# Kernel optimization log

Measured on AMD Instinct MI355X. Metric: run time of the kernel, lower is better.

## Reference

```python
import jax, jax.numpy as jnp
import numpy as np

B, S, D = 2, 2048, 1024
H, DH = 16, 64
EPS = 1e-5

def setup_inputs() -> dict:
    key = jax.random.key(0)
    ks = jax.random.split(key, 8)
    s = 0.02
    return {
        "x": jax.random.normal(ks[0], (B, S, D), dtype=jnp.float32),
        "ln_gamma": jnp.ones((D,), jnp.float32),
        "ln_beta": jnp.zeros((D,), jnp.float32),
        "wq": jax.random.normal(ks[1], (D, H * DH), jnp.float32) * s,
        "bq": jnp.zeros((H * DH,), jnp.float32),
        "wk": jax.random.normal(ks[2], (D, H * DH), jnp.float32) * s,
        "bk": jnp.zeros((H * DH,), jnp.float32),
        "wv": jax.random.normal(ks[3], (D, H * DH), jnp.float32) * s,
        "bv": jnp.zeros((H * DH,), jnp.float32),
        "wo": jax.random.normal(ks[4], (H * DH, D), jnp.float32) * s,
        "bo": jnp.zeros((D,), jnp.float32),
    }

def reference(x, ln_gamma, ln_beta, wq, bq, wk, bk, wv, bv, wo, bo):
    # Pre-LayerNorm over d_model
    mu = jnp.mean(x, axis=-1, keepdims=True)
    var = jnp.var(x, axis=-1, keepdims=True)
    xn = (x - mu) * jax.lax.rsqrt(var + EPS) * ln_gamma + ln_beta

    b, s, _ = xn.shape
    q = (xn @ wq + bq).reshape(b, s, H, DH)
    k = (xn @ wk + bk).reshape(b, s, H, DH)
    v = (xn @ wv + bv).reshape(b, s, H, DH)

    scale = jnp.sqrt(jnp.float32(DH))
    scores = jnp.einsum('bihd,bjhd->bhij', q, k) / scale  # [b,h,s,s]
    att = jax.nn.softmax(scores, axis=-1)
    out = jnp.einsum('bhij,bjhd->bihd', att, v).reshape(b, s, H * DH)
    return out @ wo + bo
```

## Files before the change

kernel.cpp:

```cpp
#include <hip/hip_runtime.h>
#include <math.h>

#define SEQ   2048
#define DM    1024
#define NHEAD 16
#define HD    64
#define NTOK  4096
#define EPS   1e-5f
#define SCALE_C 0.18033688f

typedef __attribute__((ext_vector_type(8))) short v8s;
typedef __attribute__((ext_vector_type(4))) float v4f;
typedef unsigned short ushort_t;

#define GLOAD16(g, l) __builtin_amdgcn_global_load_lds( \
    (const __attribute__((address_space(1))) unsigned int*)(g), \
    (__attribute__((address_space(3))) unsigned int*)(l), 16, 0, 0)

__device__ __forceinline__ unsigned short f2bf(float f) {
  union { float f; unsigned u; } v; v.f = f;
  unsigned r = v.u + 0x7FFFu + ((v.u >> 16) & 1u);
  return (unsigned short)(r >> 16);
}

__device__ __forceinline__ unsigned pack2_bf16(float a, float b) {
  union { float f; unsigned u; } ua, ub;
  ua.f = a; ub.f = b;
  return __builtin_amdgcn_perm(ub.u + 0x8000u, ua.u + 0x8000u, 0x07060302u);
}

__global__ __launch_bounds__(256) void ln_kernel(
    const float* __restrict__ x, const float* __restrict__ g,
    const float* __restrict__ be, ushort_t* __restrict__ y) {
  const int row = blockIdx.x;
  const int t = threadIdx.x;
  const float4 v = ((const float4*)(x + (size_t)row * DM))[t];
  float s  = v.x + v.y + v.z + v.w;
  float ss = v.x*v.x + v.y*v.y + v.z*v.z + v.w*v.w;
  #pragma unroll
  for (int off = 32; off > 0; off >>= 1) {
    s  += __shfl_down(s,  off, 64);
    ss += __shfl_down(ss, off, 64);
  }
  __shared__ float red[8];
  __shared__ float mu_s, rs_s;
  const int wid = t >> 6, lane = t & 63;
  if (lane == 0) { red[wid] = s; red[4 + wid] = ss; }
  __syncthreads();
  if (t == 0) {
    const float S  = red[0] + red[1] + red[2] + red[3];
    const float SS = red[4] + red[5] + red[6] + red[7];
    const float mu  = S * (1.0f / DM);
    const float var = SS * (1.0f / DM) - mu * mu;
    mu_s = mu; rs_s = rsqrtf(var + EPS);
  }
  __syncthreads();
  const float mu = mu_s, r = rs_s;
  const float4 gv = ((const float4*)g)[t];
  const float4 bv = ((const float4*)be)[t];
  ushort4 o;
  o.x = f2bf((v.x - mu) * r * gv.x + bv.x);
  o.y = f2bf((v.y - mu) * r * gv.y + bv.y);
  o.z = f2bf((v.z - mu) * r * gv.z + bv.z);
  o.w = f2bf((v.w - mu) * r * gv.w + bv.w);
  *(ushort4*)(y + (size_t)row * DM + t * 4) = o;
}

__global__ __launch_bounds__(256) void wt_kernel(
    const float* __restrict__ w0, const float* __restrict__ w1,
    const float* __restrict__ w2, const float* __restrict__ w3,
    ushort_t* __restrict__ o0, ushort_t* __restrict__ o1,
    ushort_t* __restrict__ o2, ushort_t* __restrict__ o3) {
  const int z = blockIdx.z;
  const float* w = (z==0) ? w0 : (z==1) ? w1 : (z==2) ? w2 : w3;
  ushort_t* o    = (z==0) ? o0 : (z==1) ? o1 : (z==2) ? o2 : o3;
  __shared__ float tile[64][65];
  const int t = threadIdx.x;
  const int n0 = blockIdx.x * 64, k0 = blockIdx.y * 64;
  const int r = t >> 4, c4 = (t & 15) * 4;
  #pragma unroll
  for (int i = 0; i < 4; ++i) {
    const float4 v = *(const float4*)(w + (size_t)(k0 + r + i*16) * DM + n0 + c4);
    tile[r + i*16][c4 + 0] = v.x;
    tile[r + i*16][c4 + 1] = v.y;
    tile[r + i*16][c4 + 2] = v.z;
    tile[r + i*16][c4 + 3] = v.w;
  }
  __syncthreads();
  #pragma unroll
  for (int i = 0; i < 4; ++i) {
    const int n = r + i*16;
    ushort4 o4;
    o4.x = f2bf(tile[c4 + 0][n]);
    o4.y = f2bf(tile[c4 + 1][n]);
    o4.z = f2bf(tile[c4 + 2][n]);
    o4.w = f2bf(tile[c4 + 3][n]);
    *(ushort4*)(o + (size_t)(n0 + n) * DM + k0 + c4) = o4;
  }
}

__device__ __forceinline__ void gemm_main(ushort_t* lsa, ushort_t* lsb,
    const ushort_t* A, const ushort_t* WT, int m0, int n0, v4f acc[4][4]) {
  const int tid = threadIdx.x;
  const int wid = tid >> 6, lane = tid & 63;
  const int mh = (wid & 1) << 6, nh = (wid >> 1) << 6;
  const int r16 = lane & 15, quad = lane >> 4;
  const int srow = lane >> 2, sch = lane & 3;
  for (int k0 = 0; k0 < DM; k0 += 32) {
    __syncthreads();
    #pragma unroll
    for (int j = 0; j < 2; ++j) {
      const int o = wid * 2 + j;
      GLOAD16(A  + (size_t)(m0 + o*16 + srow) * DM + k0 + sch*8, lsa + o*512);
      GLOAD16(WT + (size_t)(n0 + o*16 + srow) * DM + k0 + sch*8, lsb + o*512);
    }
    __syncthreads();
    v8s af[4], bfr[4];
    #pragma unroll
    for (int i = 0; i < 4; ++i) {
      af[i]  = *(const v8s*)(lsa + (mh + i*16 + r16)*32 + quad*8);
      bfr[i] = *(const v8s*)(lsb + (nh + i*16 + r16)*32 + quad*8);
    }
    #pragma unroll
    for (int i = 0; i < 4; ++i)
      #pragma unroll
      for (int j = 0; j < 4; ++j)
        acc[i][j] = __builtin_amdgcn_mfma_f32_16x16x32_bf16(af[i], bfr[j], acc[i][j], 0, 0, 0);
  }
}

__global__ __launch_bounds__(256, 2) void gemm_qkv(const ushort_t* __restrict__ xn,
    const ushort_t* __restrict__ wtq, const ushort_t* __restrict__ wtk, const ushort_t* __restrict__ wtv,
    const float* __restrict__ bq, const float* __restrict__ bk, const float* __restrict__ bv,
    ushort_t* __restrict__ qo, ushort_t* __restrict__ ko, ushort_t* __restrict__ vto) {
  __shared__ ushort_t lsa[128*32];
  __shared__ ushort_t lsb[128*32];
  const int z = blockIdx.z;
  const ushort_t* WT = (z == 0) ? wtq : (z == 1) ? wtk : wtv;
  const float* bias  = (z == 0) ? bq  : (z == 1) ? bk  : bv;
  const int m0 = blockIdx.y * 128, n0 = blockIdx.x * 128;
  v4f acc[4][4];
  #pragma unroll
  for (int i = 0; i < 4; ++i)
    #pragma unroll
    for (int j = 0; j < 4; ++j) acc[i][j] = (v4f){0.f, 0.f, 0.f, 0.f};
  gemm_main(lsa, lsb, xn, WT, m0, n0, acc);
  const int tid = threadIdx.x, wid = tid >> 6, lane = tid & 63;
  const int mh = (wid & 1) << 6, nh = (wid >> 1) << 6;
  const int r16 = lane & 15, quad = lane >> 4;
  if (z < 2) {
    ushort_t* out = (z == 0) ? qo : ko;
    const float sc = (z == 0) ? SCALE_C : 1.0f;
    #pragma unroll
    for (int bn = 0; bn < 4; ++bn) {
      const int col = n0 + nh + bn*16 + r16;
      const float bb = bias[col];
      #pragma unroll
      for (int am = 0; am < 4; ++am) {
        const int tb = m0 + mh + am*16 + quad*4;
        #pragma unroll
        for (int r = 0; r < 4; ++r)
          out[(size_t)(tb + r) * DM + col] = f2bf((acc[am][bn][r] + bb) * sc);
      }
    }
  } else {
    #pragma unroll
    for (int bn = 0; bn < 4; ++bn) {
      const int col = n0 + nh + bn*16 + r16;
      const float bb = bias[col];
      const int h = col >> 6, d = col & 63;
      #pragma unroll
      for (int am = 0; am < 4; ++am) {
        const int tb = m0 + mh + am*16 + quad*4;
        const int b = tb >> 11, t = tb & 2047;
        ushort4 o4;
        o4.x = f2bf(acc[am][bn][0] + bb);
        o4.y = f2bf(acc[am][bn][1] + bb);
        o4.z = f2bf(acc[am][bn][2] + bb);
        o4.w = f2bf(acc[am][bn][3] + bb);
        *(ushort4*)(vto + ((size_t)(b*NHEAD + h) * HD + d) * SEQ + t) = o4;
      }
    }
  }
}

__global__ __launch_bounds__(256, 2) void gemm_out(const ushort_t* __restrict__ A,
    const ushort_t* __restrict__ WT, const float* __restrict__ bias,
    float* __restrict__ out) {
  __shared__ ushort_t lsa[128*32];
  __shared__ ushort_t lsb[128*32];
  const int m0 = blockIdx.y * 128, n0 = blockIdx.x * 128;
  v4f acc[4][4];
  #pragma unroll
  for (int i = 0; i < 4; ++i)
    #pragma unroll
    for (int j = 0; j < 4; ++j) acc[i][j] = (v4f){0.f, 0.f, 0.f, 0.f};
  gemm_main(lsa, lsb, A, WT, m0, n0, acc);
  const int tid = threadIdx.x, wid = tid >> 6, lane = tid & 63;
  const int mh = (wid & 1) << 6, nh = (wid >> 1) << 6;
  const int r16 = lane & 15, quad = lane >> 4;
  #pragma unroll
  for (int bn = 0; bn < 4; ++bn) {
    const int col = n0 + nh + bn*16 + r16;
    const float bb = bias[col];
    #pragma unroll
    for (int am = 0; am < 4; ++am) {
      const int tb = m0 + mh + am*16 + quad*4;
      #pragma unroll
      for (int r = 0; r < 4; ++r)
        out[(size_t)(tb + r) * DM + col] = acc[am][bn][r] + bb;
    }
  }
}

__global__ __launch_bounds__(256, 4) void attn_kernel(
    const ushort_t* __restrict__ Q, const ushort_t* __restrict__ K,
    const ushort_t* __restrict__ Vt, ushort_t* __restrict__ O) {
  __shared__ ushort_t kbuf[2][8*512];
  __shared__ ushort_t vbuf[2][8*512];
  __shared__ ushort_t pbuf[8*512];
  const int tid = threadIdx.x, wid = tid >> 6, lane = tid & 63;
  const int r16 = lane & 15, quad = lane >> 4;
  const int q0 = blockIdx.x * 64, bh = blockIdx.y;
  const int b = bh >> 4, h = bh & 15;
  const ushort_t* gQ = Q + (size_t)b * SEQ * DM + h * HD;
  const ushort_t* gK = K + (size_t)b * SEQ * DM + h * HD;
  const ushort_t* gV = Vt + (size_t)bh * HD * SEQ;

  auto stage = [&](int kt, int buf) {
    const int k0 = kt * 64;
    if (wid < 2) {
      #pragma unroll
      for (int j = 0; j < 4; ++j) {
        const int o = (wid & 1) * 4 + j;
        GLOAD16(gK + (size_t)(k0 + (o >> 1) * 16 + r16) * DM + (o & 1) * 32 + quad * 8,
                &kbuf[buf][o * 512]);
      }
    } else {
      #pragma unroll
      for (int j = 0; j < 4; ++j) {
        const int o = (wid & 1) * 4 + j;
        GLOAD16(gV + (size_t)((o & 3) * 16 + r16) * SEQ + k0 + (o >> 2) * 32 + quad * 8,
                &vbuf[buf][o * 512]);
      }
    }
  };

  v8s qfr[4][2];
  #pragma unroll
  for (int qa = 0; qa < 4; ++qa) {
    const ushort_t* p = gQ + (size_t)(q0 + qa*16 + r16) * DM + quad * 8;
    qfr[qa][0] = *(const v8s*)p;
    qfr[qa][1] = *(const v8s*)(p + 32);
  }
  v4f acco[4];
  #pragma unroll
  for (int i = 0; i < 4; ++i) acco[i] = (v4f){0.f, 0.f, 0.f, 0.f};
  float lrun[4] = {0.f, 0.f, 0.f, 0.f};

  const int pwoff = ((wid & 1) * 2 + (quad >> 1)) * 128 + r16 * 8 + (quad & 1) * 4;
  const int pblk0 = (wid >> 1) * 512;

  stage(0, 0);
  __syncthreads();

  for (int kt = 0; kt < SEQ / 64; ++kt) {
    const int cur = kt & 1, nxt = cur ^ 1;
    if (kt + 1 < SEQ / 64) stage(kt + 1, nxt);

    const v8s ka0 = *(const v8s*)(&kbuf[cur][(wid*2 + 0) * 512] + lane * 8);
    const v8s ka1 = *(const v8s*)(&kbuf[cur][(wid*2 + 1) * 512] + lane * 8);
    v4f sacc[4];
    #pragma unroll
    for (int qa = 0; qa < 4; ++qa) {
      sacc[qa] = (v4f){0.f, 0.f, 0.f, 0.f};
      sacc[qa] = __builtin_amdgcn_mfma_f32_16x16x32_bf16(ka0, qfr[qa][0], sacc[qa], 0, 0, 0);
      sacc[qa] = __builtin_amdgcn_mfma_f32_16x16x32_bf16(ka1, qfr[qa][1], sacc[qa], 0, 0, 0);
    }

    #pragma unroll
    for (int qa = 0; qa < 4; ++qa) {
      const float e0 = __builtin_amdgcn_exp2f(sacc[qa][0]);
      const float e1 = __builtin_amdgcn_exp2f(sacc[qa][1]);
      const float e2 = __builtin_amdgcn_exp2f(sacc[qa][2]);
      const float e3 = __builtin_amdgcn_exp2f(sacc[qa][3]);
      float ls = (e0 + e1) + (e2 + e3);
      ls += __shfl_xor(ls, 16, 64);
      ls += __shfl_xor(ls, 32, 64);
      lrun[qa] += ls;
      uint2 d2;
      d2.x = pack2_bf16(e0, e1);
      d2.y = pack2_bf16(e2, e3);
      *(uint2*)(pbuf + (qa*2) * 512 + pblk0 + pwoff) = d2;
    }

    __syncthreads();

    const v8s vf0 = *(const v8s*)(&vbuf[cur][(0*4 + wid) * 512] + lane * 8);
    const v8s vf1 = *(const v8s*)(&vbuf[cur][(1*4 + wid) * 512] + lane * 8);
    #pragma unroll
    for (int qa = 0; qa < 4; ++qa) {
      const v8s pb0 = *(const v8s*)(pbuf + (qa*2 + 0) * 512 + lane * 8);
      const v8s pb1 = *(const v8s*)(pbuf + (qa*2 + 1) * 512 + lane * 8);
      acco[qa] = __builtin_amdgcn_mfma_f32_16x16x32_bf16(vf0, pb0, acco[qa], 0, 0, 0);
      acco[qa] = __builtin_amdgcn_mfma_f32_16x16x32_bf16(vf1, pb1, acco[qa], 0, 0, 0);
    }

    __syncthreads();
  }

  float* lred = (float*)pbuf;
  if (quad == 0) {
    #pragma unroll
    for (int qa = 0; qa < 4; ++qa) lred[wid*64 + qa*16 + r16] = lrun[qa];
  }
  __syncthreads();
  ushort_t* gO = O + (size_t)b * SEQ * DM + h * HD;
  #pragma unroll
  for (int qa = 0; qa < 4; ++qa) {
    const int q = qa*16 + r16;
    const float inv = 1.f / ((lred[0*64 + q] + lred[1*64 + q]) + (lred[2*64 + q] + lred[3*64 + q]));
    ushort4 o4;
    o4.x = f2bf(acco[qa][0] * inv);
    o4.y = f2bf(acco[qa][1] * inv);
    o4.z = f2bf(acco[qa][2] * inv);
    o4.w = f2bf(acco[qa][3] * inv);
    *(ushort4*)(gO + (size_t)(q0 + q) * DM + wid*16 + quad*4) = o4;
  }
}

extern "C" void kernel_launch(void* const* d_in, const int* in_sizes, int n_in,
                              void* d_out, int out_size, void* d_ws, size_t ws_size,
                              hipStream_t stream) {
  const float* x     = (const float*)d_in[0];
  const float* gamma = (const float*)d_in[1];
  const float* beta  = (const float*)d_in[2];
  const float* wq    = (const float*)d_in[3];
  const float* bq    = (const float*)d_in[4];
  const float* wk    = (const float*)d_in[5];
  const float* bk    = (const float*)d_in[6];
  const float* wv    = (const float*)d_in[7];
  const float* bv    = (const float*)d_in[8];
  const float* wo    = (const float*)d_in[9];
  const float* bo    = (const float*)d_in[10];
  float* out = (float*)d_out;

  unsigned char* w8 = (unsigned char*)d_ws;
  const size_t MB = 1024 * 1024;
  ushort_t* xn  = (ushort_t*)(w8 + 0 * MB);
  ushort_t* qb  = (ushort_t*)(w8 + 8 * MB);
  ushort_t* kb  = (ushort_t*)(w8 + 16 * MB);
  ushort_t* vt  = (ushort_t*)(w8 + 24 * MB);
  ushort_t* wtq = (ushort_t*)(w8 + 32 * MB);
  ushort_t* wtk = (ushort_t*)(w8 + 34 * MB);
  ushort_t* wtv = (ushort_t*)(w8 + 36 * MB);
  ushort_t* wto = (ushort_t*)(w8 + 38 * MB);
  ushort_t* ob  = xn;

  ln_kernel<<<dim3(NTOK), dim3(256), 0, stream>>>(x, gamma, beta, xn);
  wt_kernel<<<dim3(16, 16, 4), dim3(256), 0, stream>>>(wq, wk, wv, wo, wtq, wtk, wtv, wto);
  gemm_qkv<<<dim3(8, 32, 3), dim3(256), 0, stream>>>(xn, wtq, wtk, wtv, bq, bk, bv, qb, kb, vt);
  attn_kernel<<<dim3(SEQ / 64, 2 * NHEAD), dim3(256), 0, stream>>>(qb, kb, vt, ob);
  gemm_out<<<dim3(8, 32, 1), dim3(256), 0, stream>>>(ob, wto, bo, out);
}
```

Measured before the change: 221.3 us.

## Merge LN and weight prep kernels, drop attention double buffering, raise GEMM occupancy

Merges the LayerNorm and weight-transpose kernels into one launch to save a kernel launch. Raises the GEMM launch-bounds occupancy hint from 2 to 3 blocks. In attention, removes K/V double buffering and loads each tile synchronously, which cuts LDS use so more blocks can be resident. The price is that global loads are no longer overlapped with compute in attention.

After: 215.9 us. -2.5%, faster.

```diff
diff --git a/kernel.cpp b/kernel.cpp
--- a/kernel.cpp
+++ b/kernel.cpp
@@ -29,73 +29,72 @@
   return __builtin_amdgcn_perm(ub.u + 0x8000u, ua.u + 0x8000u, 0x07060302u);
 }
 
-__global__ __launch_bounds__(256) void ln_kernel(
+__global__ __launch_bounds__(256) void prep_kernel(
     const float* __restrict__ x, const float* __restrict__ g,
-    const float* __restrict__ be, ushort_t* __restrict__ y) {
-  const int row = blockIdx.x;
-  const int t = threadIdx.x;
-  const float4 v = ((const float4*)(x + (size_t)row * DM))[t];
-  float s  = v.x + v.y + v.z + v.w;
-  float ss = v.x*v.x + v.y*v.y + v.z*v.z + v.w*v.w;
-  #pragma unroll
-  for (int off = 32; off > 0; off >>= 1) {
-    s  += __shfl_down(s,  off, 64);
-    ss += __shfl_down(ss, off, 64);
-  }
-  __shared__ float red[8];
-  __shared__ float mu_s, rs_s;
-  const int wid = t >> 6, lane = t & 63;
-  if (lane == 0) { red[wid] = s; red[4 + wid] = ss; }
-  __syncthreads();
-  if (t == 0) {
-    const float S  = red[0] + red[1] + red[2] + red[3];
-    const float SS = red[4] + red[5] + red[6] + red[7];
-    const float mu  = S * (1.0f / DM);
-    const float var = SS * (1.0f / DM) - mu * mu;
-    mu_s = mu; rs_s = rsqrtf(var + EPS);
-  }
-  __syncthreads();
-  const float mu = mu_s, r = rs_s;
-  const float4 gv = ((const float4*)g)[t];
-  const float4 bv = ((const float4*)be)[t];
-  ushort4 o;
-  o.x = f2bf((v.x - mu) * r * gv.x + bv.x);
-  o.y = f2bf((v.y - mu) * r * gv.y + bv.y);
-  o.z = f2bf((v.z - mu) * r * gv.z + bv.z);
-  o.w = f2bf((v.w - mu) * r * gv.w + bv.w);
-  *(ushort4*)(y + (size_t)row * DM + t * 4) = o;
-}
-
-__global__ __launch_bounds__(256) void wt_kernel(
+    const float* __restrict__ be, ushort_t* __restrict__ y,
     const float* __restrict__ w0, const float* __restrict__ w1,
     const float* __restrict__ w2, const float* __restrict__ w3,
     ushort_t* __restrict__ o0, ushort_t* __restrict__ o1,
     ushort_t* __restrict__ o2, ushort_t* __restrict__ o3) {
-  const int z = blockIdx.z;
-  const float* w = (z==0) ? w0 : (z==1) ? w1 : (z==2) ? w2 : w3;
-  ushort_t* o    = (z==0) ? o0 : (z==1) ? o1 : (z==2) ? o2 : o3;
   __shared__ float tile[64][65];
   const int t = threadIdx.x;
-  const int n0 = blockIdx.x * 64, k0 = blockIdx.y * 64;
-  const int r = t >> 4, c4 = (t & 15) * 4;
-  #pragma unroll
-  for (int i = 0; i < 4; ++i) {
-    const float4 v = *(const float4*)(w + (size_t)(k0 + r + i*16) * DM + n0 + c4);
-    tile[r + i*16][c4 + 0] = v.x;
-    tile[r + i*16][c4 + 1] = v.y;
-    tile[r + i*16][c4 + 2] = v.z;
-    tile[r + i*16][c4 + 3] = v.w;
-  }
-  __syncthreads();
-  #pragma unroll
-  for (int i = 0; i < 4; ++i) {
-    const int n = r + i*16;
-    ushort4 o4;
-    o4.x = f2bf(tile[c4 + 0][n]);
-    o4.y = f2bf(tile[c4 + 1][n]);
-    o4.z = f2bf(tile[c4 + 2][n]);
-    o4.w = f2bf(tile[c4 + 3][n]);
-    *(ushort4*)(o + (size_t)(n0 + n) * DM + k0 + c4) = o4;
+  if (blockIdx.x < NTOK) {
+    const int row = blockIdx.x;
+    const float4 v = ((const float4*)(x + (size_t)row * DM))[t];
+    float s  = v.x + v.y + v.z + v.w;
+    float ss = v.x*v.x + v.y*v.y + v.z*v.z + v.w*v.w;
+    #pragma unroll
+    for (int off = 32; off > 0; off >>= 1) {
+      s  += __shfl_down(s,  off, 64);
+      ss += __shfl_down(ss, off, 64);
+    }
+    float* red = &tile[0][0];
+    const int wid = t >> 6, lane = t & 63;
+    if (lane == 0) { red[wid] = s; red[4 + wid] = ss; }
+    __syncthreads();
+    if (t == 0) {
+      const float S  = red[0] + red[1] + red[2] + red[3];
+      const float SS = red[4] + red[5] + red[6] + red[7];
+      const float mu  = S * (1.0f / DM);
+      const float var = SS * (1.0f / DM) - mu * mu;
+      red[8] = mu; red[9] = rsqrtf(var + EPS);
+    }
+    __syncthreads();
+    const float mu = red[8], r = red[9];
+    const float4 gv = ((const float4*)g)[t];
+    const float4 bv = ((const float4*)be)[t];
+    ushort4 o;
+    o.x = f2bf((v.x - mu) * r * gv.x + bv.x);
+    o.y = f2bf((v.y - mu) * r * gv.y + bv.y);
+    o.z = f2bf((v.z - mu) * r * gv.z + bv.z);
+    o.w = f2bf((v.w - mu) * r * gv.w + bv.w);
+    *(ushort4*)(y + (size_t)row * DM + t * 4) = o;
+  } else {
+    const int w = blockIdx.x - NTOK;
+    const int z = w >> 8;
+    const float* wp = (z==0) ? w0 : (z==1) ? w1 : (z==2) ? w2 : w3;
+    ushort_t* o    = (z==0) ? o0 : (z==1) ? o1 : (z==2) ? o2 : o3;
+    const int n0 = (w & 15) * 64, k0 = ((w >> 4) & 15) * 64;
+    const int r = t >> 4, c4 = (t & 15) * 4;
+    #pragma unroll
+    for (int i = 0; i < 4; ++i) {
+      const float4 v = *(const float4*)(wp + (size_t)(k0 + r + i*16) * DM + n0 + c4);
+      tile[r + i*16][c4 + 0] = v.x;
+      tile[r + i*16][c4 + 1] = v.y;
+      tile[r + i*16][c4 + 2] = v.z;
+      tile[r + i*16][c4 + 3] = v.w;
+    }
+    __syncthreads();
+    #pragma unroll
+    for (int i = 0; i < 4; ++i) {
+      const int n = r + i*16;
+      ushort4 o4;
+      o4.x = f2bf(tile[c4 + 0][n]);
+      o4.y = f2bf(tile[c4 + 1][n]);
+      o4.z = f2bf(tile[c4 + 2][n]);
+      o4.w = f2bf(tile[c4 + 3][n]);
+      *(ushort4*)(o + (size_t)(n0 + n) * DM + k0 + c4) = o4;
+    }
   }
 }
 
@@ -129,7 +128,7 @@
   }
 }
 
-__global__ __launch_bounds__(256, 2) void gemm_qkv(const ushort_t* __restrict__ xn,
+__global__ __launch_bounds__(256, 3) void gemm_qkv(const ushort_t* __restrict__ xn,
     const ushort_t* __restrict__ wtq, const ushort_t* __restrict__ wtk, const ushort_t* __restrict__ wtv,
     const float* __restrict__ bq, const float* __restrict__ bk, const float* __restrict__ bv,
     ushort_t* __restrict__ qo, ushort_t* __restrict__ ko, ushort_t* __restrict__ vto) {
@@ -184,7 +183,7 @@
   }
 }
 
-__global__ __launch_bounds__(256, 2) void gemm_out(const ushort_t* __restrict__ A,
+__global__ __launch_bounds__(256, 3) void gemm_out(const ushort_t* __restrict__ A,
     const ushort_t* __restrict__ WT, const float* __restrict__ bias,
     float* __restrict__ out) {
   __shared__ ushort_t lsa[128*32];
@@ -216,9 +215,10 @@
 __global__ __launch_bounds__(256, 4) void attn_kernel(
     const ushort_t* __restrict__ Q, const ushort_t* __restrict__ K,
     const ushort_t* __restrict__ Vt, ushort_t* __restrict__ O) {
-  __shared__ ushort_t kbuf[2][8*512];
-  __shared__ ushort_t vbuf[2][8*512];
+  __shared__ ushort_t kbuf[8*512];
+  __shared__ ushort_t vbuf[8*512];
   __shared__ ushort_t pbuf[8*512];
+  __shared__ float    lred[4][64];
   const int tid = threadIdx.x, wid = tid >> 6, lane = tid & 63;
   const int r16 = lane & 15, quad = lane >> 4;
   const int q0 = blockIdx.x * 64, bh = blockIdx.y;
@@ -227,25 +227,6 @@
   const ushort_t* gK = K + (size_t)b * SEQ * DM + h * HD;
   const ushort_t* gV = Vt + (size_t)bh * HD * SEQ;
 
-  auto stage = [&](int kt, int buf) {
-    const int k0 = kt * 64;
-    if (wid < 2) {
-      #pragma unroll
-      for (int j = 0; j < 4; ++j) {
-        const int o = (wid & 1) * 4 + j;
-        GLOAD16(gK + (size_t)(k0 + (o >> 1) * 16 + r16) * DM + (o & 1) * 32 + quad * 8,
-                &kbuf[buf][o * 512]);
-      }
-    } else {
-      #pragma unroll
-      for (int j = 0; j < 4; ++j) {
-        const int o = (wid & 1) * 4 + j;
-        GLOAD16(gV + (size_t)((o & 3) * 16 + r16) * SEQ + k0 + (o >> 2) * 32 + quad * 8,
-                &vbuf[buf][o * 512]);
-      }
-    }
-  };
-
   v8s qfr[4][2];
   #pragma unroll
   for (int qa = 0; qa < 4; ++qa) {
@@ -261,15 +242,28 @@
   const int pwoff = ((wid & 1) * 2 + (quad >> 1)) * 128 + r16 * 8 + (quad & 1) * 4;
   const int pblk0 = (wid >> 1) * 512;
 
-  stage(0, 0);
-  __syncthreads();
-
   for (int kt = 0; kt < SEQ / 64; ++kt) {
-    const int cur = kt & 1, nxt = cur ^ 1;
-    if (kt + 1 < SEQ / 64) stage(kt + 1, nxt);
-
-    const v8s ka0 = *(const v8s*)(&kbuf[cur][(wid*2 + 0) * 512] + lane * 8);
-    const v8s ka1 = *(const v8s*)(&kbuf[cur][(wid*2 + 1) * 512] + lane * 8);
+    const int k0 = kt * 64;
+    __syncthreads();
+    if (wid < 2) {
+      #pragma unroll
+      for (int j = 0; j < 4; ++j) {
+        const int o = (wid & 1) * 4 + j;
+        GLOAD16(gK + (size_t)(k0 + (o >> 1) * 16 + r16) * DM + (o & 1) * 32 + quad * 8,
+                kbuf + o * 512);
+      }
+    } else {
+      #pragma unroll
+      for (int j = 0; j < 4; ++j) {
+        const int o = (wid & 1) * 4 + j;
+        GLOAD16(gV + (size_t)((o & 3) * 16 + r16) * SEQ + k0 + (o >> 2) * 32 + quad * 8,
+                vbuf + o * 512);
+      }
+    }
+    __syncthreads();
+
+    const v8s ka0 = *(const v8s*)(kbuf + (wid*2 + 0) * 512 + lane * 8);
+    const v8s ka1 = *(const v8s*)(kbuf + (wid*2 + 1) * 512 + lane * 8);
     v4f sacc[4];
     #pragma unroll
     for (int qa = 0; qa < 4; ++qa) {
@@ -296,8 +290,8 @@
 
     __syncthreads();
 
-    const v8s vf0 = *(const v8s*)(&vbuf[cur][(0*4 + wid) * 512] + lane * 8);
-    const v8s vf1 = *(const v8s*)(&vbuf[cur][(1*4 + wid) * 512] + lane * 8);
+    const v8s vf0 = *(const v8s*)(vbuf + (0*4 + wid) * 512 + lane * 8);
+    const v8s vf1 = *(const v8s*)(vbuf + (1*4 + wid) * 512 + lane * 8);
     #pragma unroll
     for (int qa = 0; qa < 4; ++qa) {
       const v8s pb0 = *(const v8s*)(pbuf + (qa*2 + 0) * 512 + lane * 8);
@@ -305,21 +299,18 @@
       acco[qa] = __builtin_amdgcn_mfma_f32_16x16x32_bf16(vf0, pb0, acco[qa], 0, 0, 0);
       acco[qa] = __builtin_amdgcn_mfma_f32_16x16x32_bf16(vf1, pb1, acco[qa], 0, 0, 0);
     }
-
-    __syncthreads();
-  }
-
-  float* lred = (float*)pbuf;
+  }
+
   if (quad == 0) {
     #pragma unroll
-    for (int qa = 0; qa < 4; ++qa) lred[wid*64 + qa*16 + r16] = lrun[qa];
+    for (int qa = 0; qa < 4; ++qa) lred[wid][qa*16 + r16] = lrun[qa];
   }
   __syncthreads();
   ushort_t* gO = O + (size_t)b * SEQ * DM + h * HD;
   #pragma unroll
   for (int qa = 0; qa < 4; ++qa) {
     const int q = qa*16 + r16;
-    const float inv = 1.f / ((lred[0*64 + q] + lred[1*64 + q]) + (lred[2*64 + q] + lred[3*64 + q]));
+    const float inv = 1.f / ((lred[0][q] + lred[1][q]) + (lred[2][q] + lred[3][q]));
     ushort4 o4;
     o4.x = f2bf(acco[qa][0] * inv);
     o4.y = f2bf(acco[qa][1] * inv);
@@ -357,8 +348,8 @@
   ushort_t* wto = (ushort_t*)(w8 + 38 * MB);
   ushort_t* ob  = xn;
 
-  ln_kernel<<<dim3(NTOK), dim3(256), 0, stream>>>(x, gamma, beta, xn);
-  wt_kernel<<<dim3(16, 16, 4), dim3(256), 0, stream>>>(wq, wk, wv, wo, wtq, wtk, wtv, wto);
+  prep_kernel<<<dim3(NTOK + 1024), dim3(256), 0, stream>>>(
+      x, gamma, beta, xn, wq, wk, wv, wo, wtq, wtk, wtv, wto);
   gemm_qkv<<<dim3(8, 32, 3), dim3(256), 0, stream>>>(xn, wtq, wtk, wtv, bq, bk, bv, qb, kb, vt);
   attn_kernel<<<dim3(SEQ / 64, 2 * NHEAD), dim3(256), 0, stream>>>(qb, kb, vt, ob);
   gemm_out<<<dim3(8, 32, 1), dim3(256), 0, stream>>>(ob, wto, bo, out);
```
